# Kernel tuning notes

Hardware: AMD Instinct MI355X
Metric: run time of the kernel (lower is better)

The kernel has to match this reference:

```python
import jax, jax.numpy as jnp
import numpy as np

EPS = 1e-3  # keras LayerNormalization default epsilon

def layernorm(x, gamma, beta):
    mu = jnp.mean(x, axis=-1, keepdims=True)
    var = jnp.var(x, axis=-1, keepdims=True)
    return (x - mu) * jax.lax.rsqrt(var + EPS) * gamma + beta

def setup_inputs() -> dict:
    key = jax.random.key(0)
    ks = jax.random.split(key, 20)
    B, N, T, Dimg, H = 512, 100, 14, 2048, 768
    s = lambda k, *sh: jax.random.normal(k, sh, dtype=jnp.float32) * 0.02
    return {
        "img_feat": jax.random.normal(ks[0], (B, N, Dimg), dtype=jnp.float32),
        "ques_feat": jax.random.normal(ks[1], (B, T, H), dtype=jnp.float32),
        "Wc": s(ks[2], Dimg, H), "bc": jnp.zeros((H,), jnp.float32),
        "Wq": s(ks[3], H, H),    "bq": jnp.zeros((H,), jnp.float32),
        "Wi": s(ks[4], Dimg, H), "bi": jnp.zeros((H,), jnp.float32),
        "wqa": s(ks[5], H, 1), "bqa": jnp.zeros((1,), jnp.float32),
        "wia": s(ks[6], H, 1), "bia": jnp.zeros((1,), jnp.float32),
        "g1": jnp.ones((N,), jnp.float32), "b1": jnp.zeros((N,), jnp.float32),
        "g2": jnp.ones((H,), jnp.float32), "b2": jnp.zeros((H,), jnp.float32),
        "g3": jnp.ones((T,), jnp.float32), "b3": jnp.zeros((T,), jnp.float32),
        "g4": jnp.ones((H,), jnp.float32), "b4": jnp.zeros((H,), jnp.float32),
        "g5": jnp.ones((N,), jnp.float32), "b5": jnp.zeros((N,), jnp.float32),
    }

def reference(img_feat, ques_feat, Wc, bc, Wq, bq, Wi, bi, wqa, bqa, wia, bia,
              g1, b1, g2, b2, g3, b3, g4, b4, g5, b5):
    # img_feat: [B,N,Dimg], ques_feat: [B,T,H]
    img_corr = img_feat @ Wc + bc                                   # [B,N,H]
    wm = jnp.einsum('bth,bnh->btn', ques_feat, img_corr)            # [B,T,N]
    wm = jax.nn.relu(layernorm(wm, g1, b1))
    ques_embed = ques_feat @ Wq + bq                                # [B,T,H]
    img_embed = img_feat @ Wi + bi                                  # [B,N,H]
    transform_img = jnp.einsum('btn,bnh->bth', wm, img_embed)       # [B,T,H]
    ques_atten_sum = jax.nn.relu(layernorm(transform_img + ques_embed, g2, b2))
    # dropout is identity at inference
    ques_atten = (ques_atten_sum @ wqa + bqa)[..., 0]               # [B,T]
    ques_atten = jax.nn.softmax(layernorm(ques_atten, g3, b3), axis=-1)
    transform_ques = jnp.einsum('btn,bth->bnh', wm, ques_embed)     # [B,N,H]
    img_atten_sum = jax.nn.relu(layernorm(transform_ques + img_embed, g4, b4))
    img_atten = (img_atten_sum @ wia + bia)[..., 0]                 # [B,N]
    img_atten = jax.nn.softmax(layernorm(img_atten, g5, b5), axis=-1)
    ques_atten_feat = jnp.einsum('bt,bth->bh', ques_atten, ques_feat)  # [B,H]
    img_atten_feat = jnp.einsum('bn,bnd->bd', img_atten, img_feat)     # [B,Dimg]
    return (img_atten_feat, ques_atten_feat)
```

## Files before the change

### kernel.cpp

```cpp
#include <hip/hip_runtime.h>

using f32x4     = __attribute__((ext_vector_type(4))) float;
using bf16x8    = __attribute__((ext_vector_type(8))) short;
using ushort8_t = __attribute__((ext_vector_type(8))) unsigned short;

__device__ __forceinline__ unsigned short f2bf(float f) {
    unsigned u = __builtin_bit_cast(unsigned, f);
    u += 0x7fffu + ((u >> 16) & 1u);
    return (unsigned short)(u >> 16);
}
__device__ __forceinline__ float bf2f(unsigned short h) {
    return __builtin_bit_cast(float, (unsigned)h << 16);
}

__device__ __forceinline__ float wave_sum(float v) {
#pragma unroll
    for (int off = 32; off > 0; off >>= 1) v += __shfl_xor(v, off, 64);
    return v;
}
__device__ __forceinline__ float wave_max(float v) {
#pragma unroll
    for (int off = 32; off > 0; off >>= 1) v = fmaxf(v, __shfl_xor(v, off, 64));
    return v;
}

#define GLP(p)  ((const __attribute__((address_space(1))) void*)(p))
#define LDSP(p) ((__attribute__((address_space(3))) void*)(p))

__global__ __launch_bounds__(256) void cvt_bf16(const float* __restrict__ in,
                                                unsigned short* __restrict__ out, long n8) {
    long i = (long)blockIdx.x * 256 + threadIdx.x;
    long stride = (long)gridDim.x * 256;
    for (; i < n8; i += stride) {
        const float4* p = (const float4*)(in + i * 8);
        float4 a = p[0], b = p[1];
        ushort8_t v;
        v[0] = f2bf(a.x); v[1] = f2bf(a.y); v[2] = f2bf(a.z); v[3] = f2bf(a.w);
        v[4] = f2bf(b.x); v[5] = f2bf(b.y); v[6] = f2bf(b.z); v[7] = f2bf(b.w);
        *(ushort8_t*)(out + i * 8) = v;
    }
}

__global__ __launch_bounds__(256) void pack_t(
    const float* __restrict__ S0, const float* __restrict__ S1, int nsplit,
    unsigned short* __restrict__ D, int K)
{
    __shared__ float t[64][65];
    const int k0 = blockIdx.x * 64, n0 = blockIdx.y * 64;
    const float* S = (n0 < nsplit) ? S0 : S1;
    const int nb = (n0 < nsplit) ? n0 : n0 - nsplit;
    const int c = threadIdx.x & 63, r4 = threadIdx.x >> 6;
#pragma unroll
    for (int it = 0; it < 16; ++it) {
        int r = it * 4 + r4;
        t[r][c] = S[(size_t)(k0 + r) * nsplit + nb + c];
    }
    __syncthreads();
#pragma unroll
    for (int it = 0; it < 16; ++it) {
        int rn = it * 4 + r4;
        D[(size_t)(n0 + rn) * K + k0 + c] = f2bf(t[c][rn]);
    }
}

template <int OUTBF>
__global__ __launch_bounds__(512, 1) void gemm8(
    const unsigned short* __restrict__ A, const unsigned short* __restrict__ Bt,
    const float* __restrict__ bias0, const float* __restrict__ bias1, int nsplit,
    void* __restrict__ Cv, int N, int K, int NTN)
{
    __shared__ unsigned short LA[2][2][8192];
    __shared__ unsigned short LB[2][2][8192];
    const int tid = threadIdx.x, lane = tid & 63, wid = tid >> 6;

    int nwg = (int)gridDim.x, bid = (int)blockIdx.x;
    if ((nwg & 7) == 0) { int cpx = nwg >> 3; bid = (bid & 7) * cpx + (bid >> 3); }
    const int tn = bid % NTN, tm = bid / NTN;
    const size_t m0 = (size_t)tm * 256, n0 = (size_t)tn * 256;
    const int NT = K >> 6;
    const int NIT = NT >> 1;

    const int wr = wid >> 2, wc = wid & 3;
    const int hb = wc >> 1;
    const int fr = lane & 15, fs = lane >> 4;

    const int r0 = tid >> 3, s0 = ((tid & 7) - r0) & 7;
    const int r1 = r0 + 64,  s1 = ((tid & 7) - r1) & 7;
    const unsigned short* pA[2][2];
    const unsigned short* pB[2][2];
#pragma unroll
    for (int h = 0; h < 2; ++h) {
        pA[h][0] = A  + (m0 + h * 128 + r0) * K + s0 * 8;
        pA[h][1] = A  + (m0 + h * 128 + r1) * K + s1 * 8;
        pB[h][0] = Bt + (n0 + h * 128 + r0) * K + s0 * 8;
        pB[h][1] = Bt + (n0 + h * 128 + r1) * K + s1 * 8;
    }
    const int d0 = tid * 8, d1 = (tid + 512) * 8;

#define STG_A(h, t, B_) do { \
    __builtin_amdgcn_global_load_lds(GLP(pA[h][0] + (size_t)(t) * 64), LDSP(&LA[B_][h][d0]), 16, 0, 0); \
    __builtin_amdgcn_global_load_lds(GLP(pA[h][1] + (size_t)(t) * 64), LDSP(&LA[B_][h][d1]), 16, 0, 0); \
} while (0)
#define STG_B(h, t, B_) do { \
    __builtin_amdgcn_global_load_lds(GLP(pB[h][0] + (size_t)(t) * 64), LDSP(&LB[B_][h][d0]), 16, 0, 0); \
    __builtin_amdgcn_global_load_lds(GLP(pB[h][1] + (size_t)(t) * 64), LDSP(&LB[B_][h][d1]), 16, 0, 0); \
} while (0)

    int offA[2][4], offB[2][2];
#pragma unroll
    for (int mq = 0; mq < 2; ++mq)
#pragma unroll
        for (int mfl = 0; mfl < 4; ++mfl) {
            int r = mq * 64 + mfl * 16 + fr;
            offA[mq][mfl] = r * 64 + ((fs + r) & 7) * 8;
        }
#pragma unroll
    for (int nq = 0; nq < 2; ++nq)
#pragma unroll
        for (int nfl = 0; nfl < 2; ++nfl) {
            int r = (wc & 1) * 64 + nq * 32 + nfl * 16 + fr;
            offB[nq][nfl] = r * 64 + ((fs + r) & 7) * 8;
        }

#define LDA_SUB(B_, mq) do { \
    _Pragma("unroll") \
    for (int mfl = 0; mfl < 4; ++mfl) { \
        av[mfl][0] = *(const bf16x8*)&LA[B_][wr][offA[mq][mfl]]; \
        av[mfl][1] = *(const bf16x8*)&LA[B_][wr][offA[mq][mfl] ^ 32]; \
    } } while (0)
#define LDB_SUB(B_, nq, bv) do { \
    _Pragma("unroll") \
    for (int nfl = 0; nfl < 2; ++nfl) { \
        bv[nfl][0] = *(const bf16x8*)&LB[B_][hb][offB[nq][nfl]]; \
        bv[nfl][1] = *(const bf16x8*)&LB[B_][hb][offB[nq][nfl] ^ 32]; \
    } } while (0)
#define MMA_Q(mq, nq, bv) do { \
    _Pragma("unroll") \
    for (int ks = 0; ks < 2; ++ks) \
    _Pragma("unroll") \
    for (int mfl = 0; mfl < 4; ++mfl) \
    _Pragma("unroll") \
    for (int nfl = 0; nfl < 2; ++nfl) \
        acc[mq * 4 + mfl][nq * 2 + nfl] = __builtin_amdgcn_mfma_f32_16x16x32_bf16( \
            av[mfl][ks], bv[nfl][ks], acc[mq * 4 + mfl][nq * 2 + nfl], 0, 0, 0); \
    } while (0)
#define BAR  __builtin_amdgcn_s_barrier()
#define SCB  __builtin_amdgcn_sched_barrier(0)
#define LGKM0 do { asm volatile("s_waitcnt lgkmcnt(0)" ::: "memory"); SCB; } while (0)
#define PRIO1 __builtin_amdgcn_s_setprio(1)
#define PRIO0 __builtin_amdgcn_s_setprio(0)

    f32x4 acc[8][4];
#pragma unroll
    for (int i = 0; i < 8; ++i)
#pragma unroll
        for (int j = 0; j < 4; ++j) acc[i][j] = (f32x4){0.f, 0.f, 0.f, 0.f};

    STG_A(0, 0, 0); STG_A(1, 0, 0); STG_B(0, 0, 0); STG_B(1, 0, 0);
    STG_B(0, 1, 1); STG_B(1, 1, 1); STG_A(0, 1, 1);
    asm volatile("s_waitcnt vmcnt(6)" ::: "memory");
    SCB; BAR;

    for (int i = 0; i < NIT; ++i) {
        const int t0 = 2 * i, t1 = 2 * i + 1;
        const bool st = (i + 1 < NIT);
        bf16x8 av[4][2], bv0[2][2], bv1[2][2];

        LDA_SUB(0, 0); LDB_SUB(0, 0, bv0);
        STG_A(1, t1, 1);
        BAR; LGKM0;
        PRIO1; MMA_Q(0, 0, bv0); PRIO0;
        BAR;

        LDB_SUB(0, 1, bv1);
        BAR; LGKM0;
        PRIO1; MMA_Q(0, 1, bv1); PRIO0;
        BAR;

        LDA_SUB(0, 1);
        if (st) STG_B(0, t0 + 2, 0);
        BAR; LGKM0;
        PRIO1; MMA_Q(1, 1, bv1); PRIO0;
        BAR;

        if (st) { STG_B(1, t0 + 2, 0); STG_A(0, t0 + 2, 0); }
        BAR;
        PRIO1; MMA_Q(1, 0, bv0); PRIO0;
        if (st) asm volatile("s_waitcnt vmcnt(6)" ::: "memory");
        else    asm volatile("s_waitcnt vmcnt(0)" ::: "memory");
        SCB; BAR;

        LDA_SUB(1, 0); LDB_SUB(1, 0, bv0);
        if (st) STG_A(1, t0 + 2, 0);
        BAR; LGKM0;
        PRIO1; MMA_Q(0, 0, bv0); PRIO0;
        BAR;

        LDB_SUB(1, 1, bv1);
        BAR; LGKM0;
        PRIO1; MMA_Q(0, 1, bv1); PRIO0;
        BAR;

        LDA_SUB(1, 1);
        if (st) STG_B(0, t1 + 2, 1);
        BAR; LGKM0;
        PRIO1; MMA_Q(1, 1, bv1); PRIO0;
        BAR;

        if (st) { STG_B(1, t1 + 2, 1); STG_A(0, t1 + 2, 1); }
        BAR;
        PRIO1; MMA_Q(1, 0, bv0); PRIO0;
        if (st) asm volatile("s_waitcnt vmcnt(6)" ::: "memory");
        else    asm volatile("s_waitcnt vmcnt(0)" ::: "memory");
        SCB; BAR;
    }

#undef STG_A
#undef STG_B
#undef LDA_SUB
#undef LDB_SUB
#undef MMA_Q
#undef BAR
#undef SCB
#undef LGKM0
#undef PRIO1
#undef PRIO0

    const int wm = wr * 128, wn = wc * 64;
#pragma unroll
    for (int nf = 0; nf < 4; ++nf) {
        int col = (int)n0 + wn + nf * 16 + fr;
        float bs = (col < nsplit) ? bias0[col] : bias1[col - nsplit];
#pragma unroll
        for (int mf = 0; mf < 8; ++mf) {
            size_t rowb = m0 + wm + mf * 16 + fs * 4;
#pragma unroll
            for (int r = 0; r < 4; ++r) {
                float v = acc[mf][nf][r] + bs;
                if (OUTBF) ((unsigned short*)Cv)[(rowb + r) * N + col] = f2bf(v);
                else       ((float*)Cv)[(rowb + r) * N + col] = v;
            }
        }
    }
}

__global__ __launch_bounds__(256) void fused_kernel(
    const float* __restrict__ qf_g, const unsigned short* __restrict__ qbf,
    const unsigned short* __restrict__ qe_g, const unsigned short* __restrict__ imgCE,
    const unsigned short* __restrict__ imf_bf,
    const float* __restrict__ g1, const float* __restrict__ b1,
    const float* __restrict__ g2, const float* __restrict__ b2,
    const float* __restrict__ g3, const float* __restrict__ b3,
    const float* __restrict__ g4, const float* __restrict__ b4,
    const float* __restrict__ g5, const float* __restrict__ b5,
    const float* __restrict__ wqa, const float* __restrict__ bqa,
    const float* __restrict__ wia, const float* __restrict__ bia,
    float* __restrict__ out_i, float* __restrict__ out_q)
{
    const int b = blockIdx.x, tid = threadIdx.x, lane = tid & 63, wid = tid >> 6;
    __shared__ float buf[14 * 768];
    __shared__ float wms[14 * 100];
    __shared__ float red[4][28];
    __shared__ float mu_s[14], rs_s[14], qa_s[14], qw_s[14];
    __shared__ float mu2_s[10], rs2_s[10];
    __shared__ float ia_s[100], iw_s[100];

    {
        const ushort8_t* src = (const ushort8_t*)(qbf + (size_t)b * 14 * 768);
        for (int i = tid; i < 14 * 768 / 8; i += 256) {
            ushort8_t v = src[i];
#pragma unroll
            for (int j = 0; j < 8; ++j) buf[i * 8 + j] = bf2f(v[j]);
        }
    }
    __syncthreads();
    for (int n = wid; n < 100; n += 4) {
        const unsigned short* row = imgCE + ((size_t)b * 100 + n) * 1536;
        float r[12];
#pragma unroll
        for (int j = 0; j < 12; ++j) r[j] = bf2f(row[lane + 64 * j]);
        for (int t = 0; t < 14; ++t) {
            const float* q = buf + t * 768;
            float s = 0.f;
#pragma unroll
            for (int j = 0; j < 12; ++j) s = fmaf(r[j], q[lane + 64 * j], s);
            s = wave_sum(s);
            if (lane == 0) wms[t * 100 + n] = s;
        }
    }
    __syncthreads();
    for (int t = wid; t < 14; t += 4) {
        float x0 = wms[t * 100 + lane];
        float x1 = (lane + 64 < 100) ? wms[t * 100 + lane + 64] : 0.f;
        float s = wave_sum(x0 + x1);
        float q = wave_sum(x0 * x0 + x1 * x1);
        float mu = s * (1.f / 100.f);
        float var = q * (1.f / 100.f) - mu * mu;
        float rs = rsqrtf(var + 1e-3f);
        {
            float v = (x0 - mu) * rs * g1[lane] + b1[lane];
            wms[t * 100 + lane] = v > 0.f ? v : 0.f;
        }
        if (lane + 64 < 100) {
            float v = (x1 - mu) * rs * g1[lane + 64] + b1[lane + 64];
            wms[t * 100 + lane + 64] = v > 0.f ? v : 0.f;
        }
    }
    {
        const ushort8_t* src = (const ushort8_t*)(qe_g + (size_t)b * 14 * 768);
        for (int i = tid; i < 14 * 768 / 8; i += 256) {
            ushort8_t v = src[i];
#pragma unroll
            for (int j = 0; j < 8; ++j) buf[i * 8 + j] = bf2f(v[j]);
        }
    }
    __syncthreads();

    {
        float a0[14], a1[14], a2[14];
#pragma unroll
        for (int t = 0; t < 14; ++t) { a0[t] = 0.f; a1[t] = 0.f; a2[t] = 0.f; }

        const unsigned short* ie_base = imgCE + (size_t)b * 100 * 1536 + 768;
        float e0n = bf2f(ie_base[tid]), e1n = bf2f(ie_base[tid + 256]), e2n = bf2f(ie_base[tid + 512]);
        for (int n = 0; n < 100; ++n) {
            float e0 = e0n, e1 = e1n, e2 = e2n;
            if (n < 99) {
                const unsigned short* ie = ie_base + (size_t)(n + 1) * 1536;
                e0n = bf2f(ie[tid]); e1n = bf2f(ie[tid + 256]); e2n = bf2f(ie[tid + 512]);
            }
#pragma unroll
            for (int t = 0; t < 14; ++t) {
                float w = wms[t * 100 + n];
                a0[t] = fmaf(w, e0, a0[t]); a1[t] = fmaf(w, e1, a1[t]); a2[t] = fmaf(w, e2, a2[t]);
            }
        }
#pragma unroll
        for (int t = 0; t < 14; ++t) {
            a0[t] += buf[t * 768 + tid];
            a1[t] += buf[t * 768 + tid + 256];
            a2[t] += buf[t * 768 + tid + 512];
        }
#pragma unroll
        for (int t = 0; t < 14; ++t) {
            float s = wave_sum(a0[t] + a1[t] + a2[t]);
            float q = wave_sum(a0[t] * a0[t] + a1[t] * a1[t] + a2[t] * a2[t]);
            if (lane == 0) { red[wid][t] = s; red[wid][14 + t] = q; }
        }
        __syncthreads();
        if (tid < 14) {
            float s = red[0][tid] + red[1][tid] + red[2][tid] + red[3][tid];
            float q = red[0][14 + tid] + red[1][14 + tid] + red[2][14 + tid] + red[3][14 + tid];
            float mu = s * (1.f / 768.f);
            float var = q * (1.f / 768.f) - mu * mu;
            mu_s[tid] = mu; rs_s[tid] = rsqrtf(var + 1e-3f);
        }
        __syncthreads();

        float ga = g2[tid], ba = b2[tid], gb = g2[tid + 256], bb = b2[tid + 256],
              gc = g2[tid + 512], bc_ = b2[tid + 512];
        float w0 = wqa[tid], w1 = wqa[tid + 256], w2 = wqa[tid + 512];
#pragma unroll
        for (int t = 0; t < 14; ++t) {
            float mu = mu_s[t], rs = rs_s[t];
            float v0 = fmaxf((a0[t] - mu) * rs * ga + ba, 0.f);
            float v1 = fmaxf((a1[t] - mu) * rs * gb + bb, 0.f);
            float v2 = fmaxf((a2[t] - mu) * rs * gc + bc_, 0.f);
            float p = wave_sum(v0 * w0 + v1 * w1 + v2 * w2);
            if (lane == 0) red[wid][t] = p;
        }
        __syncthreads();
        if (tid < 14) qa_s[tid] = red[0][tid] + red[1][tid] + red[2][tid] + red[3][tid] + bqa[0];
        __syncthreads();
        if (tid == 0) {
            float s = 0.f;
            for (int t = 0; t < 14; ++t) s += qa_s[t];
            float mu = s * (1.f / 14.f);
            float q = 0.f;
            for (int t = 0; t < 14; ++t) { float d = qa_s[t] - mu; q += d * d; }
            float rs = rsqrtf(q * (1.f / 14.f) + 1e-3f);
            float e[14], mx = -1e30f;
            for (int t = 0; t < 14; ++t) { e[t] = (qa_s[t] - mu) * rs * g3[t] + b3[t]; mx = fmaxf(mx, e[t]); }
            float se = 0.f;
            for (int t = 0; t < 14; ++t) { e[t] = expf(e[t] - mx); se += e[t]; }
            float inv = 1.f / se;
            for (int t = 0; t < 14; ++t) qw_s[t] = e[t] * inv;
        }
        __syncthreads();

        const float* qf = qf_g + (size_t)b * 14 * 768;
#pragma unroll
        for (int c = 0; c < 3; ++c) {
            int h = tid + c * 256;
            float o = 0.f;
#pragma unroll
            for (int t = 0; t < 14; ++t) o = fmaf(qw_s[t], qf[t * 768 + h], o);
            out_q[(size_t)b * 768 + h] = o;
        }
    }
    __syncthreads();

    {
        float g4a = g4[tid], b4a = b4[tid], g4b = g4[tid + 256], b4b = b4[tid + 256],
              g4c = g4[tid + 512], b4c = b4[tid + 512];
        float wa = wia[tid], wb = wia[tid + 256], wc_ = wia[tid + 512];

        for (int g = 0; g < 10; ++g) {
            float ge0[10], ge1[10], ge2[10];
#pragma unroll
            for (int i = 0; i < 10; ++i) {
                const unsigned short* ie = imgCE + ((size_t)b * 100 + g * 10 + i) * 1536 + 768;
                ge0[i] = bf2f(ie[tid]); ge1[i] = bf2f(ie[tid + 256]); ge2[i] = bf2f(ie[tid + 512]);
            }
            float t0[10], t1[10], t2[10];
#pragma unroll
            for (int i = 0; i < 10; ++i) { t0[i] = 0.f; t1[i] = 0.f; t2[i] = 0.f; }
#pragma unroll
            for (int t = 0; t < 14; ++t) {
                float q0 = buf[t * 768 + tid], q1 = buf[t * 768 + tid + 256], q2 = buf[t * 768 + tid + 512];
#pragma unroll
                for (int i = 0; i < 10; ++i) {
                    float w = wms[t * 100 + g * 10 + i];
                    t0[i] = fmaf(w, q0, t0[i]); t1[i] = fmaf(w, q1, t1[i]); t2[i] = fmaf(w, q2, t2[i]);
                }
            }
#pragma unroll
            for (int i = 0; i < 10; ++i) {
                t0[i] += ge0[i]; t1[i] += ge1[i]; t2[i] += ge2[i];
                float s = wave_sum(t0[i] + t1[i] + t2[i]);
                float q = wave_sum(t0[i] * t0[i] + t1[i] * t1[i] + t2[i] * t2[i]);
                if (lane == 0) { red[wid][i] = s; red[wid][10 + i] = q; }
            }
            __syncthreads();
            if (tid < 10) {
                float s = red[0][tid] + red[1][tid] + red[2][tid] + red[3][tid];
                float q = red[0][10 + tid] + red[1][10 + tid] + red[2][10 + tid] + red[3][10 + tid];
                float mu = s * (1.f / 768.f);
                float var = q * (1.f / 768.f) - mu * mu;
                mu2_s[tid] = mu; rs2_s[tid] = rsqrtf(var + 1e-3f);
            }
            __syncthreads();
#pragma unroll
            for (int i = 0; i < 10; ++i) {
                float mu = mu2_s[i], rs = rs2_s[i];
                float v0 = fmaxf((t0[i] - mu) * rs * g4a + b4a, 0.f);
                float v1 = fmaxf((t1[i] - mu) * rs * g4b + b4b, 0.f);
                float v2 = fmaxf((t2[i] - mu) * rs * g4c + b4c, 0.f);
                float p = wave_sum(v0 * wa + v1 * wb + v2 * wc_);
                if (lane == 0) red[wid][i] = p;
            }
            __syncthreads();
            if (tid < 10) ia_s[g * 10 + tid] = red[0][tid] + red[1][tid] + red[2][tid] + red[3][tid] + bia[0];
            __syncthreads();
        }

        if (wid == 0) {
            float x0 = ia_s[lane];
            float x1 = (lane + 64 < 100) ? ia_s[lane + 64] : 0.f;
            float s = wave_sum(x0 + x1);
            float q = wave_sum(x0 * x0 + x1 * x1);
            float mu = s * 0.01f;
            float var = q * 0.01f - mu * mu;
            float rs = rsqrtf(var + 1e-3f);
            float v0 = (x0 - mu) * rs * g5[lane] + b5[lane];
            float v1 = (lane + 64 < 100) ? (x1 - mu) * rs * g5[lane + 64] + b5[lane + 64] : -1e30f;
            float mx = wave_max(fmaxf(v0, v1));
            float e0 = expf(v0 - mx);
            float e1 = (lane + 64 < 100) ? expf(v1 - mx) : 0.f;
            float se = wave_sum(e0 + e1);
            float inv = 1.f / se;
            iw_s[lane] = e0 * inv;
            if (lane + 64 < 100) iw_s[lane + 64] = e1 * inv;
        }
        __syncthreads();

        const unsigned short* imf = imf_bf + (size_t)b * 100 * 2048;
        float acc8[8];
#pragma unroll
        for (int j = 0; j < 8; ++j) acc8[j] = 0.f;
        for (int n = 0; n < 100; ++n) {
            ushort8_t v = *(const ushort8_t*)(imf + (size_t)n * 2048 + tid * 8);
            float w = iw_s[n];
#pragma unroll
            for (int j = 0; j < 8; ++j) acc8[j] = fmaf(w, bf2f(v[j]), acc8[j]);
        }
        float4* dst = (float4*)(out_i + (size_t)b * 2048);
        float4 oA = {acc8[0], acc8[1], acc8[2], acc8[3]};
        float4 oB = {acc8[4], acc8[5], acc8[6], acc8[7]};
        dst[tid * 2] = oA; dst[tid * 2 + 1] = oB;
    }
}

extern "C" void kernel_launch(void* const* d_in, const int* in_sizes, int n_in,
                              void* d_out, int out_size, void* d_ws, size_t ws_size,
                              hipStream_t stream)
{
    const float* img_feat = (const float*)d_in[0];
    const float* ques_feat = (const float*)d_in[1];
    const float* Wc = (const float*)d_in[2];
    const float* bc = (const float*)d_in[3];
    const float* Wq = (const float*)d_in[4];
    const float* bq = (const float*)d_in[5];
    const float* Wi = (const float*)d_in[6];
    const float* bi = (const float*)d_in[7];
    const float* wqa = (const float*)d_in[8];
    const float* bqa = (const float*)d_in[9];
    const float* wia = (const float*)d_in[10];
    const float* bia = (const float*)d_in[11];
    const float* g1 = (const float*)d_in[12]; const float* b1 = (const float*)d_in[13];
    const float* g2 = (const float*)d_in[14]; const float* b2 = (const float*)d_in[15];
    const float* g3 = (const float*)d_in[16]; const float* b3 = (const float*)d_in[17];
    const float* g4 = (const float*)d_in[18]; const float* b4 = (const float*)d_in[19];
    const float* g5 = (const float*)d_in[20]; const float* b5 = (const float*)d_in[21];

    const size_t SZ_WP   = 1536u * 2048u * 2u;
    const size_t SZ_WQT  = 768u * 768u * 2u;
    const size_t SZ_IMG  = 51200ull * 1536u * 2u;
    const size_t SZ_QE   = 7168u * 768u * 4u;
    const size_t SZ_WM   = 512u * 1400u * 4u;
    const size_t SZ_ABF  = 51200ull * 2048u * 2u;
    const size_t SZ_QBF  = 7168u * 768u * 2u;

    const size_t OFF_WP  = 0;
    const size_t OFF_WQT = OFF_WP + SZ_WP;
    const size_t OFF_IMG = OFF_WQT + SZ_WQT;
    const size_t OFF_QE  = OFF_IMG + SZ_IMG;
    const size_t OFF_WM  = OFF_QE + SZ_QE;
    const size_t OFF_ABF = OFF_WM + SZ_WM;
    const size_t OFF_QBF = OFF_ABF + SZ_ABF;
    const size_t NEED    = OFF_QBF + SZ_QBF;
    if (ws_size < NEED) return;

    char* ws = (char*)d_ws;
    unsigned short* Wp    = (unsigned short*)(ws + OFF_WP);
    unsigned short* Wqt   = (unsigned short*)(ws + OFF_WQT);
    unsigned short* imgCE = (unsigned short*)(ws + OFF_IMG);
    unsigned short* qe    = (unsigned short*)(ws + OFF_QE);
    unsigned short* Abf   = (unsigned short*)(ws + OFF_ABF);
    unsigned short* Qbf   = (unsigned short*)(ws + OFF_QBF);

    float* out_img = (float*)d_out;
    float* out_q   = (float*)d_out + 512 * 2048;

    hipLaunchKernelGGL(pack_t, dim3(32, 24), dim3(256), 0, stream, Wc, Wi, 768, Wp, 2048);
    hipLaunchKernelGGL(pack_t, dim3(12, 12), dim3(256), 0, stream, Wq, Wq, 768, Wqt, 768);
    hipLaunchKernelGGL(cvt_bf16, dim3(2048), dim3(256), 0, stream,
                       img_feat, Abf, (long)(51200ull * 2048u / 8u));
    hipLaunchKernelGGL(cvt_bf16, dim3(1024), dim3(256), 0, stream,
                       ques_feat, Qbf, (long)(7168u * 768u / 8u));

    hipLaunchKernelGGL(HIP_KERNEL_NAME(gemm8<1>), dim3(1200), dim3(512), 0, stream,
                       Abf, Wp, bc, bi, 768, (void*)imgCE, 1536, 2048, 6);
    hipLaunchKernelGGL(HIP_KERNEL_NAME(gemm8<1>), dim3(84), dim3(512), 0, stream,
                       Qbf, Wqt, bq, bq, 768, (void*)qe, 768, 768, 3);

    hipLaunchKernelGGL(fused_kernel, dim3(512), dim3(256), 0, stream,
                       ques_feat, Qbf, qe, imgCE, Abf,
                       g1, b1, g2, b2, g3, b3, g4, b4, g5, b5,
                       wqa, bqa, wia, bia, out_img, out_q);
}
```

Measured before the change: 764.5 us.

## Merge conversion and GEMM launches, split fused kernel into two roles per batch

Merges the two bf16 conversion kernels into one launch and the two GEMMs into one grouped launch, which removes launch gaps and the tail of the small GEMM. The fused kernel now runs two blocks per batch element, one for the question branch and one for the image branch. Both blocks recompute the shared wm attention matrix. The LDS buffer is stored as bf16 to halve shared memory, and image rows are prefetched one step ahead in registers. The cost is redundant wm computation and an extra bf16-to-float conversion on every LDS read.

```diff
diff --git a/kernel.cpp b/kernel.cpp
--- a/kernel.cpp
+++ b/kernel.cpp
@@ -27,10 +27,19 @@
 #define GLP(p)  ((const __attribute__((address_space(1))) void*)(p))
 #define LDSP(p) ((__attribute__((address_space(3))) void*)(p))
 
-__global__ __launch_bounds__(256) void cvt_bf16(const float* __restrict__ in,
-                                                unsigned short* __restrict__ out, long n8) {
-    long i = (long)blockIdx.x * 256 + threadIdx.x;
-    long stride = (long)gridDim.x * 256;
+__global__ __launch_bounds__(256) void cvt2(
+    const float* __restrict__ in0, unsigned short* __restrict__ out0, long n80,
+    const float* __restrict__ in1, unsigned short* __restrict__ out1, long n81, int split)
+{
+    const float* in; unsigned short* out; long n8, i, stride;
+    if ((int)blockIdx.x < split) {
+        in = in0; out = out0; n8 = n80;
+        i = (long)blockIdx.x * 256 + threadIdx.x; stride = (long)split * 256;
+    } else {
+        in = in1; out = out1; n8 = n81;
+        i = (long)(blockIdx.x - split) * 256 + threadIdx.x;
+        stride = (long)(gridDim.x - split) * 256;
+    }
     for (; i < n8; i += stride) {
         const float4* p = (const float4*)(in + i * 8);
         float4 a = p[0], b = p[1];
@@ -63,11 +72,13 @@
     }
 }
 
-template <int OUTBF>
 __global__ __launch_bounds__(512, 1) void gemm8(
-    const unsigned short* __restrict__ A, const unsigned short* __restrict__ Bt,
-    const float* __restrict__ bias0, const float* __restrict__ bias1, int nsplit,
-    void* __restrict__ Cv, int N, int K, int NTN)
+    const unsigned short* __restrict__ A1, const unsigned short* __restrict__ Bt1,
+    const float* __restrict__ b1a, const float* __restrict__ b1b, int ns1,
+    unsigned short* __restrict__ C1, int N1, int K1, int NTN1, int nblk1,
+    const unsigned short* __restrict__ A2, const unsigned short* __restrict__ Bt2,
+    const float* __restrict__ b2a, unsigned short* __restrict__ C2,
+    int N2, int K2, int NTN2, int nblk2)
 {
     __shared__ unsigned short LA[2][2][8192];
     __shared__ unsigned short LB[2][2][8192];
@@ -75,6 +86,17 @@
 
     int nwg = (int)gridDim.x, bid = (int)blockIdx.x;
     if ((nwg & 7) == 0) { int cpx = nwg >> 3; bid = (bid & 7) * cpx + (bid >> 3); }
+    const unsigned short *A, *Bt; const float *bias0, *bias1;
+    int nsplit, N, K, NTN; unsigned short* C;
+    if (bid < nblk1) {
+        A = A1; Bt = Bt1; bias0 = b1a; bias1 = b1b; nsplit = ns1;
+        C = C1; N = N1; K = K1; NTN = NTN1;
+    } else {
+        bid -= nblk1;
+        if (bid >= nblk2) return;
+        A = A2; Bt = Bt2; bias0 = b2a; bias1 = b2a; nsplit = N2;
+        C = C2; N = N2; K = K2; NTN = NTN2;
+    }
     const int tn = bid % NTN, tm = bid / NTN;
     const size_t m0 = (size_t)tm * 256, n0 = (size_t)tn * 256;
     const int NT = K >> 6;
@@ -235,11 +257,8 @@
         for (int mf = 0; mf < 8; ++mf) {
             size_t rowb = m0 + wm + mf * 16 + fs * 4;
 #pragma unroll
-            for (int r = 0; r < 4; ++r) {
-                float v = acc[mf][nf][r] + bs;
-                if (OUTBF) ((unsigned short*)Cv)[(rowb + r) * N + col] = f2bf(v);
-                else       ((float*)Cv)[(rowb + r) * N + col] = v;
-            }
+            for (int r = 0; r < 4; ++r)
+                C[(rowb + r) * N + col] = f2bf(acc[mf][nf][r] + bs);
         }
     }
 }
@@ -257,8 +276,9 @@
     const float* __restrict__ wia, const float* __restrict__ bia,
     float* __restrict__ out_i, float* __restrict__ out_q)
 {
-    const int b = blockIdx.x, tid = threadIdx.x, lane = tid & 63, wid = tid >> 6;
-    __shared__ float buf[14 * 768];
+    const int b = blockIdx.x >> 1, role = blockIdx.x & 1;
+    const int tid = threadIdx.x, lane = tid & 63, wid = tid >> 6;
+    __shared__ unsigned short buf[14 * 768];
     __shared__ float wms[14 * 100];
     __shared__ float red[4][28];
     __shared__ float mu_s[14], rs_s[14], qa_s[14], qw_s[14];
@@ -267,25 +287,32 @@
 
     {
         const ushort8_t* src = (const ushort8_t*)(qbf + (size_t)b * 14 * 768);
-        for (int i = tid; i < 14 * 768 / 8; i += 256) {
-            ushort8_t v = src[i];
-#pragma unroll
-            for (int j = 0; j < 8; ++j) buf[i * 8 + j] = bf2f(v[j]);
-        }
+        for (int i = tid; i < 14 * 768 / 8; i += 256) *(ushort8_t*)&buf[i * 8] = src[i];
     }
     __syncthreads();
-    for (int n = wid; n < 100; n += 4) {
-        const unsigned short* row = imgCE + ((size_t)b * 100 + n) * 1536;
-        float r[12];
-#pragma unroll
-        for (int j = 0; j < 12; ++j) r[j] = bf2f(row[lane + 64 * j]);
-        for (int t = 0; t < 14; ++t) {
-            const float* q = buf + t * 768;
-            float s = 0.f;
-#pragma unroll
-            for (int j = 0; j < 12; ++j) s = fmaf(r[j], q[lane + 64 * j], s);
-            s = wave_sum(s);
-            if (lane == 0) wms[t * 100 + n] = s;
+    {
+        float rcur[12], rnxt[12];
+        {
+            const unsigned short* row = imgCE + ((size_t)b * 100 + wid) * 1536;
+#pragma unroll
+            for (int j = 0; j < 12; ++j) rnxt[j] = bf2f(row[lane + 64 * j]);
+        }
+        for (int n = wid; n < 100; n += 4) {
+#pragma unroll
+            for (int j = 0; j < 12; ++j) rcur[j] = rnxt[j];
+            if (n + 4 < 100) {
+                const unsigned short* row = imgCE + ((size_t)b * 100 + n + 4) * 1536;
+#pragma unroll
+                for (int j = 0; j < 12; ++j) rnxt[j] = bf2f(row[lane + 64 * j]);
+            }
+            for (int t = 0; t < 14; ++t) {
+                const unsigned short* q = buf + t * 768;
+                float s = 0.f;
+#pragma unroll
+                for (int j = 0; j < 12; ++j) s = fmaf(rcur[j], bf2f(q[lane + 64 * j]), s);
+                s = wave_sum(s);
+                if (lane == 0) wms[t * 100 + n] = s;
+            }
         }
     }
     __syncthreads();
@@ -308,15 +335,11 @@
     }
     {
         const ushort8_t* src = (const ushort8_t*)(qe_g + (size_t)b * 14 * 768);
-        for (int i = tid; i < 14 * 768 / 8; i += 256) {
-            ushort8_t v = src[i];
-#pragma unroll
-            for (int j = 0; j < 8; ++j) buf[i * 8 + j] = bf2f(v[j]);
-        }
+        for (int i = tid; i < 14 * 768 / 8; i += 256) *(ushort8_t*)&buf[i * 8] = src[i];
     }
     __syncthreads();
 
-    {
+    if (role == 0) {
         float a0[14], a1[14], a2[14];
 #pragma unroll
         for (int t = 0; t < 14; ++t) { a0[t] = 0.f; a1[t] = 0.f; a2[t] = 0.f; }
@@ -337,9 +360,9 @@
         }
 #pragma unroll
         for (int t = 0; t < 14; ++t) {
-            a0[t] += buf[t * 768 + tid];
-            a1[t] += buf[t * 768 + tid + 256];
-            a2[t] += buf[t * 768 + tid + 512];
+            a0[t] += bf2f(buf[t * 768 + tid]);
+            a1[t] += bf2f(buf[t * 768 + tid + 256]);
+            a2[t] += bf2f(buf[t * 768 + tid + 512]);
         }
 #pragma unroll
         for (int t = 0; t < 14; ++t) {
@@ -397,10 +420,7 @@
             for (int t = 0; t < 14; ++t) o = fmaf(qw_s[t], qf[t * 768 + h], o);
             out_q[(size_t)b * 768 + h] = o;
         }
-    }
-    __syncthreads();
-
-    {
+    } else {
         float g4a = g4[tid], b4a = b4[tid], g4b = g4[tid + 256], b4b = b4[tid + 256],
               g4c = g4[tid + 512], b4c = b4[tid + 512];
         float wa = wia[tid], wb = wia[tid + 256], wc_ = wia[tid + 512];
@@ -417,7 +437,8 @@
             for (int i = 0; i < 10; ++i) { t0[i] = 0.f; t1[i] = 0.f; t2[i] = 0.f; }
 #pragma unroll
             for (int t = 0; t < 14; ++t) {
-                float q0 = buf[t * 768 + tid], q1 = buf[t * 768 + tid + 256], q2 = buf[t * 768 + tid + 512];
+                float q0 = bf2f(buf[t * 768 + tid]), q1 = bf2f(buf[t * 768 + tid + 256]),
+                      q2 = bf2f(buf[t * 768 + tid + 512]);
 #pragma unroll
                 for (int i = 0; i < 10; ++i) {
                     float w = wms[t * 100 + g * 10 + i];
@@ -544,17 +565,15 @@
 
     hipLaunchKernelGGL(pack_t, dim3(32, 24), dim3(256), 0, stream, Wc, Wi, 768, Wp, 2048);
     hipLaunchKernelGGL(pack_t, dim3(12, 12), dim3(256), 0, stream, Wq, Wq, 768, Wqt, 768);
-    hipLaunchKernelGGL(cvt_bf16, dim3(2048), dim3(256), 0, stream,
-                       img_feat, Abf, (long)(51200ull * 2048u / 8u));
-    hipLaunchKernelGGL(cvt_bf16, dim3(1024), dim3(256), 0, stream,
-                       ques_feat, Qbf, (long)(7168u * 768u / 8u));
-
-    hipLaunchKernelGGL(HIP_KERNEL_NAME(gemm8<1>), dim3(1200), dim3(512), 0, stream,
-                       Abf, Wp, bc, bi, 768, (void*)imgCE, 1536, 2048, 6);
-    hipLaunchKernelGGL(HIP_KERNEL_NAME(gemm8<1>), dim3(84), dim3(512), 0, stream,
-                       Qbf, Wqt, bq, bq, 768, (void*)qe, 768, 768, 3);
-
-    hipLaunchKernelGGL(fused_kernel, dim3(512), dim3(256), 0, stream,
+    hipLaunchKernelGGL(cvt2, dim3(2304), dim3(256), 0, stream,
+                       img_feat, Abf, (long)(51200ull * 2048u / 8u),
+                       ques_feat, Qbf, (long)(7168u * 768u / 8u), 2048);
+
+    hipLaunchKernelGGL(gemm8, dim3(1288), dim3(512), 0, stream,
+                       Abf, Wp, bc, bi, 768, imgCE, 1536, 2048, 6, 1200,
+                       Qbf, Wqt, bq, qe, 768, 768, 3, 84);
+
+    hipLaunchKernelGGL(fused_kernel, dim3(1024), dim3(256), 0, stream,
                        ques_feat, Qbf, qe, imgCE, Abf,
                        g1, b1, g2, b2, g3, b3, g4, b4, g5, b5,
                        wqa, bqa, wia, bia, out_img, out_q);
```

Result: slower. 907.6 us (+18.7%).
